# Optimization experiments

Hardware: AMD Instinct MI355X
Metric: run time of the kernel (lower is better)

## Reference

```python
import jax, jax.numpy as jnp
import numpy as np

B, S, D, H = 2, 2048, 512, 8
DH = D // H  # depth per head = 64
MAX_SEQ = 2048


def setup_inputs() -> dict:
    key = jax.random.key(0)
    ks = jax.random.split(key, 12)
    sc = 1.0 / np.sqrt(D)
    inp = {
        "v": jax.random.normal(ks[0], (B, S, D), jnp.float32),
        "k": jax.random.normal(ks[1], (B, S, D), jnp.float32),
        "q": jax.random.normal(ks[2], (B, S, D), jnp.float32),
        # causal look-ahead mask: 1.0 where attention is disallowed (j > i)
        "mask": jnp.triu(jnp.ones((S, S), jnp.float32), k=1)[None, None, :, :],
        "Wq": jax.random.normal(ks[3], (D, D), jnp.float32) * sc,
        "bq": jnp.zeros((D,), jnp.float32),
        "Wk": jax.random.normal(ks[4], (D, D), jnp.float32) * sc,
        "bk": jnp.zeros((D,), jnp.float32),
        "Wv": jax.random.normal(ks[5], (D, D), jnp.float32) * sc,
        "bv": jnp.zeros((D,), jnp.float32),
        "Wo": jax.random.normal(ks[6], (D, D), jnp.float32) * sc,
        "bo": jnp.zeros((D,), jnp.float32),
        # relative position embedding table [max_seq, depth]
        "E": jax.random.normal(ks[7], (MAX_SEQ, DH), jnp.float32) * 0.02,
    }
    return inp


def reference(v, k, q, mask, Wq, bq, Wk, bk, Wv, bv, Wo, bo, E):
    b, s, d = q.shape
    split = lambda x: x.reshape(b, s, H, DH).transpose(0, 2, 1, 3)  # [b,h,s,dh]
    qh = split(q @ Wq + bq)
    kh = split(k @ Wk + bk)
    vh = split(v @ Wv + bv)

    # QK^T logits [b,h,lq,lk]
    logits = jnp.einsum("bhqd,bhkd->bhqk", qh, kh)

    # relative position bias (Music Transformer skewing trick)
    Eq = E[max(MAX_SEQ - s, 0):, :]          # left embedding slice [s, dh]
    m = Eq.shape[0]
    QE = jnp.einsum("bhld,md->bhlm", qh, Eq)  # [b,h,s,m]
    # keep entries where col >= m-1-row (qe masking)
    rows = jnp.arange(s)[:, None]
    cols = jnp.arange(m)[None, :]
    QE = QE * (cols >= (m - 1 - rows)).astype(QE.dtype)
    # skew: pad one zero column on the left, reshape, drop first row
    padded = jnp.pad(QE, ((0, 0), (0, 0), (0, 0), (1, 0)))  # [b,h,s,m+1]
    Srel = padded.reshape(b, H, m + 1, s)[:, :, 1:, :]       # [b,h,m,s]
    # here len_q == len_k == s, so Srel is [b,h,s,s] with no extra pad/slice

    logits = (logits + Srel) / jnp.sqrt(jnp.float32(DH))
    logits = logits + mask * -1e9
    attn = jax.nn.softmax(logits, axis=-1)
    out = jnp.einsum("bhqk,bhkd->bhqd", attn, vh)
    out = out.transpose(0, 2, 1, 3).reshape(b, s, d)
    return out @ Wo + bo, attn
```

## Files before the change

### kernel.cpp

```cpp
#include <hip/hip_runtime.h>

typedef __bf16 bf16x8 __attribute__((ext_vector_type(8)));
typedef float f32x4 __attribute__((ext_vector_type(4)));

#define MFMA(a, b, c) __builtin_amdgcn_mfma_f32_16x16x32_bf16((a), (b), (c), 0, 0, 0)

__global__ __launch_bounds__(256)
void prep_kernel(const float* __restrict__ Wq, const float* __restrict__ Wk,
                 const float* __restrict__ Wv, const float* __restrict__ Wo,
                 const float* __restrict__ E,
                 __bf16* __restrict__ WT, __bf16* __restrict__ Ebf)
{
    __shared__ float tl[32][33];
    const int bx = blockIdx.x, t = threadIdx.x;
    if (bx < 1024) {
        const int wi = bx >> 8, tile = bx & 255;
        const float* W = wi == 0 ? Wq : wi == 1 ? Wk : wi == 2 ? Wv : Wo;
        __bf16* dst = WT + (size_t)wi * 512 * 512;
        const int k0 = (tile >> 4) << 5, n0 = (tile & 15) << 5;
        const int tx = t & 31, ty = t >> 5;
        #pragma unroll
        for (int i = 0; i < 4; ++i) {
            int r = ty + i * 8;
            tl[r][tx] = W[(size_t)(k0 + r) * 512 + n0 + tx];
        }
        __syncthreads();
        #pragma unroll
        for (int i = 0; i < 4; ++i) {
            int r = ty + i * 8;
            dst[(size_t)(n0 + r) * 512 + k0 + tx] = (__bf16)tl[tx][r];
        }
    } else {
        int idx = (bx - 1024) * 256 + t;
        for (int i = idx; i < 2048 * 64; i += 8 * 256)
            Ebf[i] = (__bf16)E[i];
    }
}

__global__ __launch_bounds__(256, 2)
void proj_kernel(const float* __restrict__ xq, const float* __restrict__ xk,
                 const float* __restrict__ xv, const __bf16* __restrict__ WT,
                 const float* __restrict__ bq, const float* __restrict__ bk,
                 const float* __restrict__ bv,
                 __bf16* __restrict__ outQ, __bf16* __restrict__ outK,
                 __bf16* __restrict__ outV)
{
    __shared__ __bf16 As[64][72];
    __shared__ __bf16 Bs[64][72];
    const int t = threadIdx.x;
    const int z = blockIdx.y;
    const float* x = z == 0 ? xq : z == 1 ? xk : xv;
    const float* bias = z == 0 ? bq : z == 1 ? bk : bv;
    const __bf16* Wt = WT + (size_t)z * (512 * 512);
    __bf16* outp = z == 0 ? outQ : z == 1 ? outK : outV;

    const int bx = blockIdx.x;
    const int m0 = (bx >> 3) << 6;
    const int n0 = (bx & 7) << 6;
    const int w = t >> 6, lane = t & 63, quad = lane >> 4, l16 = lane & 15;

    f32x4 acc[4];
    #pragma unroll
    for (int i = 0; i < 4; ++i) acc[i] = (f32x4)0.f;

    for (int k0 = 0; k0 < 512; k0 += 64) {
        __syncthreads();
        {
            int r = t >> 2, c0 = (t & 3) << 4;
            const float4* src = (const float4*)(x + (size_t)(m0 + r) * 512 + k0 + c0);
            float fa[16];
            *(float4*)&fa[0]  = src[0];
            *(float4*)&fa[4]  = src[1];
            *(float4*)&fa[8]  = src[2];
            *(float4*)&fa[12] = src[3];
            __bf16 tb[16];
            #pragma unroll
            for (int j = 0; j < 16; ++j) tb[j] = (__bf16)fa[j];
            *(int4*)&As[r][c0]     = *(int4*)&tb[0];
            *(int4*)&As[r][c0 + 8] = *(int4*)&tb[8];
            const int4* bsrc = (const int4*)(Wt + (size_t)(n0 + r) * 512 + k0 + c0);
            int4 b0 = bsrc[0], b1 = bsrc[1];
            *(int4*)&Bs[r][c0]     = b0;
            *(int4*)&Bs[r][c0 + 8] = b1;
        }
        __syncthreads();
        bf16x8 a0 = *(const bf16x8*)&As[(w << 4) + l16][quad * 8];
        bf16x8 a1 = *(const bf16x8*)&As[(w << 4) + l16][32 + quad * 8];
        #pragma unroll
        for (int nt = 0; nt < 4; ++nt) {
            bf16x8 b0 = *(const bf16x8*)&Bs[nt * 16 + l16][quad * 8];
            bf16x8 b1 = *(const bf16x8*)&Bs[nt * 16 + l16][32 + quad * 8];
            acc[nt] = MFMA(a0, b0, acc[nt]);
            acc[nt] = MFMA(a1, b1, acc[nt]);
        }
    }
    #pragma unroll
    for (int nt = 0; nt < 4; ++nt) {
        const int n = n0 + nt * 16 + l16;
        const float bb = bias[n];
        const int h = n >> 6, dh = n & 63;
        #pragma unroll
        for (int i = 0; i < 4; ++i) {
            const int m = m0 + (w << 4) + quad * 4 + i;
            const int b = m >> 11, s = m & 2047;
            outp[(((size_t)(b * 8 + h) * 2048 + s) << 6) + dh] = (__bf16)(acc[nt][i] + bb);
        }
    }
}

__global__ __launch_bounds__(256, 2)
void attn_kernel(const __bf16* __restrict__ Qh, const __bf16* __restrict__ Kh,
                 const __bf16* __restrict__ Vh, const __bf16* __restrict__ Eb,
                 float* __restrict__ attn, __bf16* __restrict__ ctx)
{
    __shared__ __bf16 Qs[64][72];
    __shared__ __bf16 Ks[64][72];
    __shared__ __bf16 Vs[64][72];
    __shared__ __bf16 Es[128][72];

    const int t = threadIdx.x;
    const int bx = blockIdx.x;
    const int tt = bx & 31;
    const int bh = ((bx & 255) >> 5) + ((bx >> 8) << 3);
    const int q0 = (bx < 256 ? (31 - tt) : tt) << 6;
    const int w = t >> 6, lane = t & 63, quad = lane >> 4, l16 = lane & 15;
    const int qw = w << 4;

    const __bf16* Qg = Qh + (size_t)bh * (2048 * 64);
    const __bf16* Kg = Kh + (size_t)bh * (2048 * 64);
    const __bf16* Vg = Vh + (size_t)bh * (2048 * 64);
    float* attng = attn + (size_t)bh * (2048 * 2048);

    {
        int r = t >> 2, c0 = (t & 3) << 4;
        const int4* src = (const int4*)(Qg + (size_t)(q0 + r) * 64 + c0);
        int4 v0 = src[0], v1 = src[1];
        *(int4*)&Qs[r][c0]     = v0;
        *(int4*)&Qs[r][c0 + 8] = v1;
    }
    __syncthreads();
    const bf16x8 qa0 = *(const bf16x8*)&Qs[qw + l16][quad * 8];
    const bf16x8 qa1 = *(const bf16x8*)&Qs[qw + l16][32 + quad * 8];
    __syncthreads();

    __bf16 (* const Ps)[72] = Qs;

    const int kr = t >> 2, kc = (t & 3) << 4;
    const int er = t >> 1, ec = (t & 1) << 5;

    int4 kreg0, kreg1, ereg0, ereg1, ereg2, ereg3, vreg0, vreg1;

    const int nkt = (q0 >> 6) + 1;

    float lsum[4] = {0.f, 0.f, 0.f, 0.f}, linv[4];
    f32x4 acc_o[4];
    #pragma unroll
    for (int i = 0; i < 4; ++i) acc_o[i] = (f32x4)0.f;

    {
        const int4* ks = (const int4*)(Kg + (size_t)kr * 64 + kc);
        kreg0 = ks[0]; kreg1 = ks[1];
        int e = 1984 - q0 + er; if (e > 2047) e = 2047;
        const int4* es = (const int4*)(Eb + (size_t)e * 64 + ec);
        ereg0 = es[0]; ereg1 = es[1]; ereg2 = es[2]; ereg3 = es[3];
    }

    for (int pass = 0; pass < 2; ++pass) {
        for (int kt = 0; kt < nkt; ++kt) {
            const int k0 = kt << 6;
            __syncthreads();
            *(int4*)&Ks[kr][kc]     = kreg0;
            *(int4*)&Ks[kr][kc + 8] = kreg1;
            *(int4*)&Es[er][ec]      = ereg0;
            *(int4*)&Es[er][ec + 8]  = ereg1;
            *(int4*)&Es[er][ec + 16] = ereg2;
            *(int4*)&Es[er][ec + 24] = ereg3;
            if (pass) {
                __bf16 tmp[16];
                *(int4*)&tmp[0] = vreg0; *(int4*)&tmp[8] = vreg1;
                #pragma unroll
                for (int j = 0; j < 16; ++j) {
                    const int dh = kc + j;
                    Vs[dh][kr ^ (((dh >> 4) & 1) << 3)] = tmp[j];
                }
            }
            __syncthreads();

            {
                int nk = kt + 1, np = pass;
                if (nk == nkt) { nk = 0; np = pass + 1; }
                if (np < 2) {
                    const int k0n = nk << 6;
                    const int4* ks = (const int4*)(Kg + (size_t)(k0n + kr) * 64 + kc);
                    kreg0 = ks[0]; kreg1 = ks[1];
                    int e = 1984 - q0 + k0n + er; if (e > 2047) e = 2047;
                    const int4* es = (const int4*)(Eb + (size_t)e * 64 + ec);
                    ereg0 = es[0]; ereg1 = es[1]; ereg2 = es[2]; ereg3 = es[3];
                    if (np == 1) {
                        const int4* vs = (const int4*)(Vg + (size_t)(k0n + kr) * 64 + kc);
                        vreg0 = vs[0]; vreg1 = vs[1];
                    }
                }
            }

            f32x4 aqk[4];
            #pragma unroll
            for (int nt = 0; nt < 4; ++nt) {
                aqk[nt] = (f32x4)0.f;
                bf16x8 b0 = *(const bf16x8*)&Ks[nt * 16 + l16][quad * 8];
                bf16x8 b1 = *(const bf16x8*)&Ks[nt * 16 + l16][32 + quad * 8];
                aqk[nt] = MFMA(qa0, b0, aqk[nt]);
                aqk[nt] = MFMA(qa1, b1, aqk[nt]);
            }
            f32x4 aqe[5];
            #pragma unroll
            for (int jj = 0; jj < 5; ++jj) {
                aqe[jj] = (f32x4)0.f;
                const int ebr = 48 - qw + jj * 16 + l16;
                bf16x8 b0 = *(const bf16x8*)&Es[ebr][quad * 8];
                bf16x8 b1 = *(const bf16x8*)&Es[ebr][32 + quad * 8];
                aqe[jj] = MFMA(qa0, b0, aqe[jj]);
                aqe[jj] = MFMA(qa1, b1, aqe[jj]);
            }

            #pragma unroll
            for (int i = 0; i < 4; ++i) {
                const int d  = quad * 4 + i;
                const int ql = qw + d;
                const int qq = q0 + ql;
                const int sp = (l16 + 15 - d) & 15;
                const bool hi = l16 > d;
                float ev[4];
                #pragma unroll
                for (int nt = 0; nt < 4; ++nt) {
                    float g0 = __shfl(aqe[nt][i], sp, 16);
                    float g1 = __shfl(aqe[nt + 1][i], sp, 16);
                    float qe = hi ? g1 : g0;
                    float s = (aqk[nt][i] + qe) * 0.125f;
                    ev[nt] = (k0 + nt * 16 + l16 <= qq) ? __expf(s) : 0.f;
                }
                if (pass == 0) {
                    lsum[i] += (ev[0] + ev[1]) + (ev[2] + ev[3]);
                } else {
                    #pragma unroll
                    for (int nt = 0; nt < 4; ++nt) {
                        float pr = ev[nt] * linv[i];
                        attng[(size_t)qq * 2048 + k0 + nt * 16 + l16] = pr;
                        Ps[ql][nt * 16 + l16] = (__bf16)pr;
                    }
                }
            }

            if (pass) {
                const bf16x8 pa0 = *(const bf16x8*)&Ps[qw + l16][quad * 8];
                const bf16x8 pa1 = *(const bf16x8*)&Ps[qw + l16][32 + quad * 8];
                #pragma unroll
                for (int dt = 0; dt < 4; ++dt) {
                    const int xr = (dt & 1) << 3;
                    bf16x8 vb0 = *(const bf16x8*)&Vs[dt * 16 + l16][(quad * 8) ^ xr];
                    bf16x8 vb1 = *(const bf16x8*)&Vs[dt * 16 + l16][32 + ((quad * 8) ^ xr)];
                    acc_o[dt] = MFMA(pa0, vb0, acc_o[dt]);
                    acc_o[dt] = MFMA(pa1, vb1, acc_o[dt]);
                }
            }
        }
        if (pass == 0) {
            #pragma unroll
            for (int i = 0; i < 4; ++i) {
                float v = lsum[i];
                #pragma unroll
                for (int m = 1; m < 16; m <<= 1) v += __shfl_xor(v, m, 16);
                linv[i] = 1.0f / v;
            }
        }
    }

    {
        const int b = bh >> 3, h = bh & 7;
        #pragma unroll
        for (int dt = 0; dt < 4; ++dt) {
            #pragma unroll
            for (int i = 0; i < 4; ++i) {
                const int qq = q0 + qw + quad * 4 + i;
                const int d = dt * 16 + l16;
                ctx[((size_t)(b * 2048 + qq) * 512) + h * 64 + d] = (__bf16)acc_o[dt][i];
            }
        }
    }
    {
        const int kend = q0 + 64;
        const int zc = 2048 - kend;
        if (zc > 0) {
            const int zq = zc >> 2;
            const float4 z4 = make_float4(0.f, 0.f, 0.f, 0.f);
            for (int idx = t; idx < 64 * zq; idx += 256) {
                int r = idx / zq, c = idx - r * zq;
                *(float4*)&attng[(size_t)(q0 + r) * 2048 + kend + c * 4] = z4;
            }
        }
    }
}

__global__ __launch_bounds__(256, 2)
void outproj_kernel(const __bf16* __restrict__ ctx, const __bf16* __restrict__ WoT,
                    const float* __restrict__ bo, float* __restrict__ out)
{
    __shared__ __bf16 As[64][72];
    __shared__ __bf16 Bs[64][72];
    const int t = threadIdx.x;
    const int bx = blockIdx.x;
    const int m0 = (bx >> 3) << 6;
    const int n0 = (bx & 7) << 6;
    const int w = t >> 6, lane = t & 63, quad = lane >> 4, l16 = lane & 15;

    f32x4 acc[4];
    #pragma unroll
    for (int i = 0; i < 4; ++i) acc[i] = (f32x4)0.f;

    for (int k0 = 0; k0 < 512; k0 += 64) {
        __syncthreads();
        {
            int r = t >> 2, c0 = (t & 3) << 4;
            const int4* asrc = (const int4*)(ctx + (size_t)(m0 + r) * 512 + k0 + c0);
            int4 a0 = asrc[0], a1 = asrc[1];
            *(int4*)&As[r][c0]     = a0;
            *(int4*)&As[r][c0 + 8] = a1;
            const int4* bsrc = (const int4*)(WoT + (size_t)(n0 + r) * 512 + k0 + c0);
            int4 b0 = bsrc[0], b1 = bsrc[1];
            *(int4*)&Bs[r][c0]     = b0;
            *(int4*)&Bs[r][c0 + 8] = b1;
        }
        __syncthreads();
        bf16x8 a0 = *(const bf16x8*)&As[(w << 4) + l16][quad * 8];
        bf16x8 a1 = *(const bf16x8*)&As[(w << 4) + l16][32 + quad * 8];
        #pragma unroll
        for (int nt = 0; nt < 4; ++nt) {
            bf16x8 b0 = *(const bf16x8*)&Bs[nt * 16 + l16][quad * 8];
            bf16x8 b1 = *(const bf16x8*)&Bs[nt * 16 + l16][32 + quad * 8];
            acc[nt] = MFMA(a0, b0, acc[nt]);
            acc[nt] = MFMA(a1, b1, acc[nt]);
        }
    }
    #pragma unroll
    for (int nt = 0; nt < 4; ++nt) {
        const int n = n0 + nt * 16 + l16;
        const float bb = bo[n];
        #pragma unroll
        for (int i = 0; i < 4; ++i) {
            const int m = m0 + (w << 4) + quad * 4 + i;
            out[(size_t)m * 512 + n] = acc[nt][i] + bb;
        }
    }
}

extern "C" void kernel_launch(void* const* d_in, const int* in_sizes, int n_in,
                              void* d_out, int out_size, void* d_ws, size_t ws_size,
                              hipStream_t stream) {
    const float* v  = (const float*)d_in[0];
    const float* k  = (const float*)d_in[1];
    const float* q  = (const float*)d_in[2];
    const float* Wq = (const float*)d_in[4];
    const float* bq = (const float*)d_in[5];
    const float* Wk = (const float*)d_in[6];
    const float* bk = (const float*)d_in[7];
    const float* Wv = (const float*)d_in[8];
    const float* bv = (const float*)d_in[9];
    const float* Wo = (const float*)d_in[10];
    const float* bo = (const float*)d_in[11];
    const float* E  = (const float*)d_in[12];

    float* out  = (float*)d_out;
    float* attn = out + (size_t)2 * 2048 * 512;

    char* ws = (char*)d_ws;
    __bf16* WT  = (__bf16*)ws;
    __bf16* Ebf = (__bf16*)(ws + (size_t)4 * 512 * 512 * 2);
    __bf16* Qh  = (__bf16*)(ws + (size_t)4 * 512 * 512 * 2 + (size_t)2048 * 64 * 2);
    __bf16* Kh  = Qh + (size_t)2 * 8 * 2048 * 64;
    __bf16* Vh  = Kh + (size_t)2 * 8 * 2048 * 64;
    __bf16* ctx = Vh + (size_t)2 * 8 * 2048 * 64;

    prep_kernel<<<1032, 256, 0, stream>>>(Wq, Wk, Wv, Wo, E, WT, Ebf);
    proj_kernel<<<dim3(512, 3), 256, 0, stream>>>(q, k, v, WT, bq, bk, bv, Qh, Kh, Vh);
    attn_kernel<<<512, 256, 0, stream>>>(Qh, Kh, Vh, Ebf, attn, ctx);
    outproj_kernel<<<512, 256, 0, stream>>>(ctx, WT + (size_t)3 * 512 * 512, bo, out);
}
```

Before: 439.0 us.

## Single-pass attention with unnormalized bf16 P buffer, separate normalize kernel, prefetching GEMMs

```diff
diff --git a/kernel.cpp b/kernel.cpp
--- a/kernel.cpp
+++ b/kernel.cpp
@@ -37,7 +37,7 @@
     }
 }
 
-__global__ __launch_bounds__(256, 2)
+__global__ __launch_bounds__(256, 3)
 void proj_kernel(const float* __restrict__ xq, const float* __restrict__ xk,
                  const float* __restrict__ xv, const __bf16* __restrict__ WT,
                  const float* __restrict__ bq, const float* __restrict__ bk,
@@ -45,7 +45,7 @@
                  __bf16* __restrict__ outQ, __bf16* __restrict__ outK,
                  __bf16* __restrict__ outV)
 {
-    __shared__ __bf16 As[64][72];
+    __shared__ __bf16 As[128][72];
     __shared__ __bf16 Bs[64][72];
     const int t = threadIdx.x;
     const int z = blockIdx.y;
@@ -55,55 +55,85 @@
     __bf16* outp = z == 0 ? outQ : z == 1 ? outK : outV;
 
     const int bx = blockIdx.x;
-    const int m0 = (bx >> 3) << 6;
+    const int m0 = (bx >> 3) << 7;
     const int n0 = (bx & 7) << 6;
     const int w = t >> 6, lane = t & 63, quad = lane >> 4, l16 = lane & 15;
 
-    f32x4 acc[4];
-    #pragma unroll
-    for (int i = 0; i < 4; ++i) acc[i] = (f32x4)0.f;
+    const int ar = t >> 1, ac = (t & 1) << 5;
+    const int br = t >> 2, bc = (t & 3) << 4;
+
+    float4 xr[8];
+    int4 wr0, wr1;
+    {
+        const float4* xs = (const float4*)(x + (size_t)(m0 + ar) * 512 + ac);
+        #pragma unroll
+        for (int j = 0; j < 8; ++j) xr[j] = xs[j];
+        const int4* wsrc = (const int4*)(Wt + (size_t)(n0 + br) * 512 + bc);
+        wr0 = wsrc[0]; wr1 = wsrc[1];
+    }
+
+    f32x4 acc[2][4];
+    #pragma unroll
+    for (int rb = 0; rb < 2; ++rb)
+        #pragma unroll
+        for (int nt = 0; nt < 4; ++nt) acc[rb][nt] = (f32x4)0.f;
 
     for (int k0 = 0; k0 < 512; k0 += 64) {
         __syncthreads();
         {
-            int r = t >> 2, c0 = (t & 3) << 4;
-            const float4* src = (const float4*)(x + (size_t)(m0 + r) * 512 + k0 + c0);
-            float fa[16];
-            *(float4*)&fa[0]  = src[0];
-            *(float4*)&fa[4]  = src[1];
-            *(float4*)&fa[8]  = src[2];
-            *(float4*)&fa[12] = src[3];
-            __bf16 tb[16];
-            #pragma unroll
-            for (int j = 0; j < 16; ++j) tb[j] = (__bf16)fa[j];
-            *(int4*)&As[r][c0]     = *(int4*)&tb[0];
-            *(int4*)&As[r][c0 + 8] = *(int4*)&tb[8];
-            const int4* bsrc = (const int4*)(Wt + (size_t)(n0 + r) * 512 + k0 + c0);
-            int4 b0 = bsrc[0], b1 = bsrc[1];
-            *(int4*)&Bs[r][c0]     = b0;
-            *(int4*)&Bs[r][c0 + 8] = b1;
-        }
-        __syncthreads();
-        bf16x8 a0 = *(const bf16x8*)&As[(w << 4) + l16][quad * 8];
-        bf16x8 a1 = *(const bf16x8*)&As[(w << 4) + l16][32 + quad * 8];
+            __bf16 tb[32];
+            #pragma unroll
+            for (int j = 0; j < 8; ++j) {
+                tb[j * 4 + 0] = (__bf16)xr[j].x;
+                tb[j * 4 + 1] = (__bf16)xr[j].y;
+                tb[j * 4 + 2] = (__bf16)xr[j].z;
+                tb[j * 4 + 3] = (__bf16)xr[j].w;
+            }
+            *(int4*)&As[ar][ac]      = ((int4*)tb)[0];
+            *(int4*)&As[ar][ac + 8]  = ((int4*)tb)[1];
+            *(int4*)&As[ar][ac + 16] = ((int4*)tb)[2];
+            *(int4*)&As[ar][ac + 24] = ((int4*)tb)[3];
+            *(int4*)&Bs[br][bc]     = wr0;
+            *(int4*)&Bs[br][bc + 8] = wr1;
+        }
+        __syncthreads();
+        if (k0 + 64 < 512) {
+            const float4* xs = (const float4*)(x + (size_t)(m0 + ar) * 512 + k0 + 64 + ac);
+            #pragma unroll
+            for (int j = 0; j < 8; ++j) xr[j] = xs[j];
+            const int4* wsrc = (const int4*)(Wt + (size_t)(n0 + br) * 512 + k0 + 64 + bc);
+            wr0 = wsrc[0]; wr1 = wsrc[1];
+        }
+        bf16x8 bf[8];
         #pragma unroll
         for (int nt = 0; nt < 4; ++nt) {
-            bf16x8 b0 = *(const bf16x8*)&Bs[nt * 16 + l16][quad * 8];
-            bf16x8 b1 = *(const bf16x8*)&Bs[nt * 16 + l16][32 + quad * 8];
-            acc[nt] = MFMA(a0, b0, acc[nt]);
-            acc[nt] = MFMA(a1, b1, acc[nt]);
-        }
-    }
-    #pragma unroll
-    for (int nt = 0; nt < 4; ++nt) {
-        const int n = n0 + nt * 16 + l16;
-        const float bb = bias[n];
-        const int h = n >> 6, dh = n & 63;
-        #pragma unroll
-        for (int i = 0; i < 4; ++i) {
-            const int m = m0 + (w << 4) + quad * 4 + i;
-            const int b = m >> 11, s = m & 2047;
-            outp[(((size_t)(b * 8 + h) * 2048 + s) << 6) + dh] = (__bf16)(acc[nt][i] + bb);
+            bf[nt * 2]     = *(const bf16x8*)&Bs[nt * 16 + l16][quad * 8];
+            bf[nt * 2 + 1] = *(const bf16x8*)&Bs[nt * 16 + l16][32 + quad * 8];
+        }
+        #pragma unroll
+        for (int rb = 0; rb < 2; ++rb) {
+            bf16x8 a0 = *(const bf16x8*)&As[w * 32 + rb * 16 + l16][quad * 8];
+            bf16x8 a1 = *(const bf16x8*)&As[w * 32 + rb * 16 + l16][32 + quad * 8];
+            #pragma unroll
+            for (int nt = 0; nt < 4; ++nt) {
+                acc[rb][nt] = MFMA(a0, bf[nt * 2], acc[rb][nt]);
+                acc[rb][nt] = MFMA(a1, bf[nt * 2 + 1], acc[rb][nt]);
+            }
+        }
+    }
+    #pragma unroll
+    for (int rb = 0; rb < 2; ++rb) {
+        #pragma unroll
+        for (int nt = 0; nt < 4; ++nt) {
+            const int n = n0 + nt * 16 + l16;
+            const float bb = bias[n];
+            const int h = n >> 6, dh = n & 63;
+            #pragma unroll
+            for (int i = 0; i < 4; ++i) {
+                const int m = m0 + w * 32 + rb * 16 + quad * 4 + i;
+                const int b = m >> 11, s = m & 2047;
+                outp[(((size_t)(b * 8 + h) * 2048 + s) << 6) + dh] = (__bf16)(acc[rb][nt][i] + bb);
+            }
         }
     }
 }
@@ -111,7 +141,8 @@
 __global__ __launch_bounds__(256, 2)
 void attn_kernel(const __bf16* __restrict__ Qh, const __bf16* __restrict__ Kh,
                  const __bf16* __restrict__ Vh, const __bf16* __restrict__ Eb,
-                 float* __restrict__ attn, __bf16* __restrict__ ctx)
+                 __bf16* __restrict__ Pout, float* __restrict__ Linv,
+                 __bf16* __restrict__ ctx)
 {
     __shared__ __bf16 Qs[64][72];
     __shared__ __bf16 Ks[64][72];
@@ -129,7 +160,7 @@
     const __bf16* Qg = Qh + (size_t)bh * (2048 * 64);
     const __bf16* Kg = Kh + (size_t)bh * (2048 * 64);
     const __bf16* Vg = Vh + (size_t)bh * (2048 * 64);
-    float* attng = attn + (size_t)bh * (2048 * 2048);
+    __bf16* Pg = Pout + (size_t)bh * (2048 * 2048);
 
     {
         int r = t >> 2, c0 = (t & 3) << 4;
@@ -152,7 +183,7 @@
 
     const int nkt = (q0 >> 6) + 1;
 
-    float lsum[4] = {0.f, 0.f, 0.f, 0.f}, linv[4];
+    float lsum[4] = {0.f, 0.f, 0.f, 0.f};
     f32x4 acc_o[4];
     #pragma unroll
     for (int i = 0; i < 4; ++i) acc_o[i] = (f32x4)0.f;
@@ -163,116 +194,103 @@
         int e = 1984 - q0 + er; if (e > 2047) e = 2047;
         const int4* es = (const int4*)(Eb + (size_t)e * 64 + ec);
         ereg0 = es[0]; ereg1 = es[1]; ereg2 = es[2]; ereg3 = es[3];
-    }
-
-    for (int pass = 0; pass < 2; ++pass) {
-        for (int kt = 0; kt < nkt; ++kt) {
-            const int k0 = kt << 6;
-            __syncthreads();
-            *(int4*)&Ks[kr][kc]     = kreg0;
-            *(int4*)&Ks[kr][kc + 8] = kreg1;
-            *(int4*)&Es[er][ec]      = ereg0;
-            *(int4*)&Es[er][ec + 8]  = ereg1;
-            *(int4*)&Es[er][ec + 16] = ereg2;
-            *(int4*)&Es[er][ec + 24] = ereg3;
-            if (pass) {
-                __bf16 tmp[16];
-                *(int4*)&tmp[0] = vreg0; *(int4*)&tmp[8] = vreg1;
-                #pragma unroll
-                for (int j = 0; j < 16; ++j) {
-                    const int dh = kc + j;
-                    Vs[dh][kr ^ (((dh >> 4) & 1) << 3)] = tmp[j];
-                }
-            }
-            __syncthreads();
-
-            {
-                int nk = kt + 1, np = pass;
-                if (nk == nkt) { nk = 0; np = pass + 1; }
-                if (np < 2) {
-                    const int k0n = nk << 6;
-                    const int4* ks = (const int4*)(Kg + (size_t)(k0n + kr) * 64 + kc);
-                    kreg0 = ks[0]; kreg1 = ks[1];
-                    int e = 1984 - q0 + k0n + er; if (e > 2047) e = 2047;
-                    const int4* es = (const int4*)(Eb + (size_t)e * 64 + ec);
-                    ereg0 = es[0]; ereg1 = es[1]; ereg2 = es[2]; ereg3 = es[3];
-                    if (np == 1) {
-                        const int4* vs = (const int4*)(Vg + (size_t)(k0n + kr) * 64 + kc);
-                        vreg0 = vs[0]; vreg1 = vs[1];
-                    }
-                }
-            }
-
-            f32x4 aqk[4];
+        const int4* vs = (const int4*)(Vg + (size_t)kr * 64 + kc);
+        vreg0 = vs[0]; vreg1 = vs[1];
+    }
+
+    const float csc = 0.125f * 1.44269504f;
+
+    for (int kt = 0; kt < nkt; ++kt) {
+        const int k0 = kt << 6;
+        __syncthreads();
+        *(int4*)&Ks[kr][kc]     = kreg0;
+        *(int4*)&Ks[kr][kc + 8] = kreg1;
+        *(int4*)&Es[er][ec]      = ereg0;
+        *(int4*)&Es[er][ec + 8]  = ereg1;
+        *(int4*)&Es[er][ec + 16] = ereg2;
+        *(int4*)&Es[er][ec + 24] = ereg3;
+        {
+            __bf16 tmp[16];
+            *(int4*)&tmp[0] = vreg0; *(int4*)&tmp[8] = vreg1;
+            #pragma unroll
+            for (int j = 0; j < 16; ++j) {
+                const int dh = kc + j;
+                Vs[dh][kr ^ (((dh >> 4) & 1) << 3)] = tmp[j];
+            }
+        }
+        __syncthreads();
+
+        if (kt + 1 < nkt) {
+            const int k0n = (kt + 1) << 6;
+            const int4* ks = (const int4*)(Kg + (size_t)(k0n + kr) * 64 + kc);
+            kreg0 = ks[0]; kreg1 = ks[1];
+            int e = 1984 - q0 + k0n + er; if (e > 2047) e = 2047;
+            const int4* es = (const int4*)(Eb + (size_t)e * 64 + ec);
+            ereg0 = es[0]; ereg1 = es[1]; ereg2 = es[2]; ereg3 = es[3];
+            const int4* vs = (const int4*)(Vg + (size_t)(k0n + kr) * 64 + kc);
+            vreg0 = vs[0]; vreg1 = vs[1];
+        }
+
+        f32x4 aqk[4];
+        #pragma unroll
+        for (int nt = 0; nt < 4; ++nt) {
+            aqk[nt] = (f32x4)0.f;
+            bf16x8 b0 = *(const bf16x8*)&Ks[nt * 16 + l16][quad * 8];
+            bf16x8 b1 = *(const bf16x8*)&Ks[nt * 16 + l16][32 + quad * 8];
+            aqk[nt] = MFMA(qa0, b0, aqk[nt]);
+            aqk[nt] = MFMA(qa1, b1, aqk[nt]);
+        }
+        f32x4 aqe[5];
+        #pragma unroll
+        for (int jj = 0; jj < 5; ++jj) {
+            aqe[jj] = (f32x4)0.f;
+            const int ebr = 48 - qw + jj * 16 + l16;
+            bf16x8 b0 = *(const bf16x8*)&Es[ebr][quad * 8];
+            bf16x8 b1 = *(const bf16x8*)&Es[ebr][32 + quad * 8];
+            aqe[jj] = MFMA(qa0, b0, aqe[jj]);
+            aqe[jj] = MFMA(qa1, b1, aqe[jj]);
+        }
+
+        #pragma unroll
+        for (int i = 0; i < 4; ++i) {
+            const int d  = quad * 4 + i;
+            const int ql = qw + d;
+            const int qq = q0 + ql;
+            const int sp = (l16 + 15 - d) & 15;
+            const bool hi = l16 > d;
             #pragma unroll
             for (int nt = 0; nt < 4; ++nt) {
-                aqk[nt] = (f32x4)0.f;
-                bf16x8 b0 = *(const bf16x8*)&Ks[nt * 16 + l16][quad * 8];
-                bf16x8 b1 = *(const bf16x8*)&Ks[nt * 16 + l16][32 + quad * 8];
-                aqk[nt] = MFMA(qa0, b0, aqk[nt]);
-                aqk[nt] = MFMA(qa1, b1, aqk[nt]);
-            }
-            f32x4 aqe[5];
-            #pragma unroll
-            for (int jj = 0; jj < 5; ++jj) {
-                aqe[jj] = (f32x4)0.f;
-                const int ebr = 48 - qw + jj * 16 + l16;
-                bf16x8 b0 = *(const bf16x8*)&Es[ebr][quad * 8];
-                bf16x8 b1 = *(const bf16x8*)&Es[ebr][32 + quad * 8];
-                aqe[jj] = MFMA(qa0, b0, aqe[jj]);
-                aqe[jj] = MFMA(qa1, b1, aqe[jj]);
-            }
-
-            #pragma unroll
-            for (int i = 0; i < 4; ++i) {
-                const int d  = quad * 4 + i;
-                const int ql = qw + d;
-                const int qq = q0 + ql;
-                const int sp = (l16 + 15 - d) & 15;
-                const bool hi = l16 > d;
-                float ev[4];
-                #pragma unroll
-                for (int nt = 0; nt < 4; ++nt) {
-                    float g0 = __shfl(aqe[nt][i], sp, 16);
-                    float g1 = __shfl(aqe[nt + 1][i], sp, 16);
-                    float qe = hi ? g1 : g0;
-                    float s = (aqk[nt][i] + qe) * 0.125f;
-                    ev[nt] = (k0 + nt * 16 + l16 <= qq) ? __expf(s) : 0.f;
-                }
-                if (pass == 0) {
-                    lsum[i] += (ev[0] + ev[1]) + (ev[2] + ev[3]);
-                } else {
-                    #pragma unroll
-                    for (int nt = 0; nt < 4; ++nt) {
-                        float pr = ev[nt] * linv[i];
-                        attng[(size_t)qq * 2048 + k0 + nt * 16 + l16] = pr;
-                        Ps[ql][nt * 16 + l16] = (__bf16)pr;
-                    }
-                }
-            }
-
-            if (pass) {
-                const bf16x8 pa0 = *(const bf16x8*)&Ps[qw + l16][quad * 8];
-                const bf16x8 pa1 = *(const bf16x8*)&Ps[qw + l16][32 + quad * 8];
-                #pragma unroll
-                for (int dt = 0; dt < 4; ++dt) {
-                    const int xr = (dt & 1) << 3;
-                    bf16x8 vb0 = *(const bf16x8*)&Vs[dt * 16 + l16][(quad * 8) ^ xr];
-                    bf16x8 vb1 = *(const bf16x8*)&Vs[dt * 16 + l16][32 + ((quad * 8) ^ xr)];
-                    acc_o[dt] = MFMA(pa0, vb0, acc_o[dt]);
-                    acc_o[dt] = MFMA(pa1, vb1, acc_o[dt]);
-                }
-            }
-        }
-        if (pass == 0) {
-            #pragma unroll
-            for (int i = 0; i < 4; ++i) {
-                float v = lsum[i];
-                #pragma unroll
-                for (int m = 1; m < 16; m <<= 1) v += __shfl_xor(v, m, 16);
-                linv[i] = 1.0f / v;
-            }
-        }
+                float g0 = __shfl(aqe[nt][i], sp, 16);
+                float g1 = __shfl(aqe[nt + 1][i], sp, 16);
+                float qe = hi ? g1 : g0;
+                float ev = (k0 + nt * 16 + l16 <= qq)
+                         ? exp2f((aqk[nt][i] + qe) * csc) : 0.f;
+                lsum[i] += ev;
+                __bf16 pb = (__bf16)ev;
+                Pg[(size_t)qq * 2048 + k0 + nt * 16 + l16] = pb;
+                Ps[ql][nt * 16 + l16] = pb;
+            }
+        }
+
+        const bf16x8 pa0 = *(const bf16x8*)&Ps[qw + l16][quad * 8];
+        const bf16x8 pa1 = *(const bf16x8*)&Ps[qw + l16][32 + quad * 8];
+        #pragma unroll
+        for (int dt = 0; dt < 4; ++dt) {
+            const int xr = (dt & 1) << 3;
+            bf16x8 vb0 = *(const bf16x8*)&Vs[dt * 16 + l16][(quad * 8) ^ xr];
+            bf16x8 vb1 = *(const bf16x8*)&Vs[dt * 16 + l16][32 + ((quad * 8) ^ xr)];
+            acc_o[dt] = MFMA(pa0, vb0, acc_o[dt]);
+            acc_o[dt] = MFMA(pa1, vb1, acc_o[dt]);
+        }
+    }
+
+    float linv[4];
+    #pragma unroll
+    for (int i = 0; i < 4; ++i) {
+        float v = lsum[i];
+        #pragma unroll
+        for (int m = 1; m < 16; m <<= 1) v += __shfl_xor(v, m, 16);
+        linv[i] = 1.0f / v;
     }
 
     {
@@ -283,21 +301,51 @@
             for (int i = 0; i < 4; ++i) {
                 const int qq = q0 + qw + quad * 4 + i;
                 const int d = dt * 16 + l16;
-                ctx[((size_t)(b * 2048 + qq) * 512) + h * 64 + d] = (__bf16)acc_o[dt][i];
-            }
-        }
-    }
-    {
-        const int kend = q0 + 64;
-        const int zc = 2048 - kend;
-        if (zc > 0) {
-            const int zq = zc >> 2;
-            const float4 z4 = make_float4(0.f, 0.f, 0.f, 0.f);
-            for (int idx = t; idx < 64 * zq; idx += 256) {
-                int r = idx / zq, c = idx - r * zq;
-                *(float4*)&attng[(size_t)(q0 + r) * 2048 + kend + c * 4] = z4;
-            }
-        }
+                ctx[((size_t)(b * 2048 + qq) * 512) + h * 64 + d] =
+                    (__bf16)(acc_o[dt][i] * linv[i]);
+            }
+        }
+    }
+    if (l16 == 0) {
+        #pragma unroll
+        for (int i = 0; i < 4; ++i)
+            Linv[(size_t)bh * 2048 + q0 + qw + quad * 4 + i] = linv[i];
+    }
+}
+
+__global__ __launch_bounds__(256)
+void norm_kernel(const __bf16* __restrict__ Pin, const float* __restrict__ Linv,
+                 float* __restrict__ attn)
+{
+    const int blk = blockIdx.x;
+    const int bh = blk >> 9;
+    const int r0 = (blk & 511) << 2;
+    const int t = threadIdx.x;
+    const int q = r0 + (t >> 6);
+    const int c0 = (t & 63) << 5;
+    const float li = Linv[(size_t)bh * 2048 + q];
+    const int qend = ((q >> 6) + 1) << 6;
+    const __bf16* prow = Pin + ((size_t)bh * 2048 + q) * 2048;
+    float* arow = attn + ((size_t)bh * 2048 + q) * 2048;
+
+    if (c0 < qend) {
+        #pragma unroll
+        for (int j = 0; j < 4; ++j) {
+            int4 raw = *(const int4*)(prow + c0 + j * 8);
+            bf16x8 pv = *(bf16x8*)&raw;
+            float4 o0, o1;
+            o0.x = (float)pv[0] * li; o0.y = (float)pv[1] * li;
+            o0.z = (float)pv[2] * li; o0.w = (float)pv[3] * li;
+            o1.x = (float)pv[4] * li; o1.y = (float)pv[5] * li;
+            o1.z = (float)pv[6] * li; o1.w = (float)pv[7] * li;
+            *(float4*)(arow + c0 + j * 8)     = o0;
+            *(float4*)(arow + c0 + j * 8 + 4) = o1;
+        }
+    } else {
+        const float4 z4 = make_float4(0.f, 0.f, 0.f, 0.f);
+        #pragma unroll
+        for (int j = 0; j < 8; ++j)
+            *(float4*)(arow + c0 + j * 4) = z4;
     }
 }
 
@@ -312,6 +360,15 @@
     const int m0 = (bx >> 3) << 6;
     const int n0 = (bx & 7) << 6;
     const int w = t >> 6, lane = t & 63, quad = lane >> 4, l16 = lane & 15;
+    const int r = t >> 2, c0 = (t & 3) << 4;
+
+    int4 ar0, ar1, br0, br1;
+    {
+        const int4* asrc = (const int4*)(ctx + (size_t)(m0 + r) * 512 + c0);
+        ar0 = asrc[0]; ar1 = asrc[1];
+        const int4* bsrc = (const int4*)(WoT + (size_t)(n0 + r) * 512 + c0);
+        br0 = bsrc[0]; br1 = bsrc[1];
+    }
 
     f32x4 acc[4];
     #pragma unroll
@@ -319,18 +376,17 @@
 
     for (int k0 = 0; k0 < 512; k0 += 64) {
         __syncthreads();
-        {
-            int r = t >> 2, c0 = (t & 3) << 4;
-            const int4* asrc = (const int4*)(ctx + (size_t)(m0 + r) * 512 + k0 + c0);
-            int4 a0 = asrc[0], a1 = asrc[1];
-            *(int4*)&As[r][c0]     = a0;
-            *(int4*)&As[r][c0 + 8] = a1;
-            const int4* bsrc = (const int4*)(WoT + (size_t)(n0 + r) * 512 + k0 + c0);
-            int4 b0 = bsrc[0], b1 = bsrc[1];
-            *(int4*)&Bs[r][c0]     = b0;
-            *(int4*)&Bs[r][c0 + 8] = b1;
-        }
-        __syncthreads();
+        *(int4*)&As[r][c0]     = ar0;
+        *(int4*)&As[r][c0 + 8] = ar1;
+        *(int4*)&Bs[r][c0]     = br0;
+        *(int4*)&Bs[r][c0 + 8] = br1;
+        __syncthreads();
+        if (k0 + 64 < 512) {
+            const int4* asrc = (const int4*)(ctx + (size_t)(m0 + r) * 512 + k0 + 64 + c0);
+            ar0 = asrc[0]; ar1 = asrc[1];
+            const int4* bsrc = (const int4*)(WoT + (size_t)(n0 + r) * 512 + k0 + 64 + c0);
+            br0 = bsrc[0]; br1 = bsrc[1];
+        }
         bf16x8 a0 = *(const bf16x8*)&As[(w << 4) + l16][quad * 8];
         bf16x8 a1 = *(const bf16x8*)&As[(w << 4) + l16][32 + quad * 8];
         #pragma unroll
@@ -373,15 +429,18 @@
     float* attn = out + (size_t)2 * 2048 * 512;
 
     char* ws = (char*)d_ws;
-    __bf16* WT  = (__bf16*)ws;
-    __bf16* Ebf = (__bf16*)(ws + (size_t)4 * 512 * 512 * 2);
-    __bf16* Qh  = (__bf16*)(ws + (size_t)4 * 512 * 512 * 2 + (size_t)2048 * 64 * 2);
-    __bf16* Kh  = Qh + (size_t)2 * 8 * 2048 * 64;
-    __bf16* Vh  = Kh + (size_t)2 * 8 * 2048 * 64;
-    __bf16* ctx = Vh + (size_t)2 * 8 * 2048 * 64;
+    __bf16* WT   = (__bf16*)ws;
+    __bf16* Ebf  = (__bf16*)(ws + (size_t)(4 * 512 * 512) * 2);
+    __bf16* Qh   = Ebf + (size_t)2048 * 64;
+    __bf16* Kh   = Qh + (size_t)16 * 2048 * 64;
+    __bf16* Vh   = Kh + (size_t)16 * 2048 * 64;
+    __bf16* ctx  = Vh + (size_t)16 * 2048 * 64;
+    __bf16* Pout = ctx + (size_t)16 * 2048 * 64;
+    float*  Linv = (float*)(Pout + (size_t)16 * 2048 * 2048);
 
     prep_kernel<<<1032, 256, 0, stream>>>(Wq, Wk, Wv, Wo, E, WT, Ebf);
-    proj_kernel<<<dim3(512, 3), 256, 0, stream>>>(q, k, v, WT, bq, bk, bv, Qh, Kh, Vh);
-    attn_kernel<<<512, 256, 0, stream>>>(Qh, Kh, Vh, Ebf, attn, ctx);
+    proj_kernel<<<dim3(256, 3), 256, 0, stream>>>(q, k, v, WT, bq, bk, bv, Qh, Kh, Vh);
+    attn_kernel<<<512, 256, 0, stream>>>(Qh, Kh, Vh, Ebf, Pout, Linv, ctx);
+    norm_kernel<<<8192, 256, 0, stream>>>(Pout, Linv, attn);
     outproj_kernel<<<512, 256, 0, stream>>>(ctx, WT + (size_t)3 * 512 * 512, bo, out);
 }
```

New measurement: 495.5 us. 1.13x slower.
